# Optimization experiments

Measured on AMD Instinct MI355X. Metric: run time of the kernel, lower is better.

The kernel has to match this reference:

```python
import jax, jax.numpy as jnp
import numpy as np


def setup_inputs() -> dict:
    key = jax.random.key(0)
    k_x, k_idx, k_sgn = jax.random.split(key, 3)
    batch, original_dim, proj_dim, c = 32, 1000000, 4096, 8
    x = jax.random.normal(k_x, (batch, original_dim), dtype=jnp.float32)
    rand_indices = jax.random.randint(k_idx, (original_dim, c), 0, proj_dim, dtype=jnp.int32)
    # random signs in {-1, +1}, matching torch.randint(0,2)*2-1 cast to int8
    rand_signs = (jax.random.randint(k_sgn, (original_dim, c), 0, 2, dtype=jnp.int32) * 2 - 1)
    return {"x": x, "rand_indices": rand_indices, "rand_signs": rand_signs,
            "proj_dim": proj_dim, "c": c}


def reference(x, rand_indices, rand_signs, proj_dim, c):
    # SJLT: each input coordinate d is scattered to c random output buckets
    # with random sign; normalized by 1/sqrt(c) so the sketch preserves norms.
    scale = jnp.asarray(1.0 / np.sqrt(c), dtype=x.dtype)
    batch = x.shape[0]
    out = jnp.zeros((batch, proj_dim), dtype=x.dtype)
    # c is a small fixed constant; loop over it, vectorize over batch & features.
    for j in range(c):
        vals = x * rand_signs[:, j].astype(x.dtype)      # [B, D]
        out = out.at[:, rand_indices[:, j]].add(vals)     # scatter-add along proj dim
    return out * scale
```

## Files before the change

### kernel.cpp

```cpp
#include <hip/hip_runtime.h>
#include <hip/hip_fp16.h>


#define D_TOTAL 1000000
#define PROJ    4096
#define C_SK    8
#define NE      (D_TOTAL * C_SK)
#define SCALE   0.35355339059327373f

#define CAPA    131072
#define CAP     2304
#define BINCAP  112
#define TILE    4096
#define NBLK_A  ((NE + TILE - 1) / TILE)
#define NBLK_T  ((D_TOTAL + 255) / 256)

#define CURA_OFF   0
#define CURB_OFF   16384
#define LISTB_OFF  65536
#define LISTB_SZ   ((size_t)PROJ * CAP * 4)
#define XT_OFF     (LISTB_OFF + LISTB_SZ)
#define XT_SZ      ((size_t)D_TOTAL * 32 * 2)
#define LISTA_OFF  (XT_OFF + XT_SZ)
#define LISTA_SZ   ((size_t)64 * CAPA * 4)
#define WS_ROOMY   (LISTA_OFF + LISTA_SZ)
#define WS_TIGHT   (XT_OFF + XT_SZ)

__global__ void init_cursors_kernel(int* __restrict__ curA, int* __restrict__ curB) {
    int i = blockIdx.x * blockDim.x + threadIdx.x;
    if (i < 64)   curA[i] = i * CAPA;
    if (i < PROJ) curB[i] = i * CAP;
}

__device__ __forceinline__ void rank_and_stage(bool ok, int kb, int payload,
                                               int* __restrict__ cnt,
                                               int* __restrict__ stage,
                                               int* __restrict__ gcur,
                                               int* __restrict__ glist,
                                               int gcur_idx, int glim) {
    const unsigned long long valid = __ballot(ok);
    unsigned long long mask = valid;
    #pragma unroll
    for (int b = 0; b < 6; ++b) {
        const unsigned long long vote = __ballot((kb >> b) & 1);
        mask &= ((kb >> b) & 1) ? vote : ~vote;
    }
    if (ok) {
        const int lane = threadIdx.x & 63;
        const int rank = __popcll(mask & ((1ULL << lane) - 1ULL));
        const int leader = __ffsll((unsigned long long)mask) - 1;
        int base = 0;
        if (rank == 0) base = atomicAdd(&cnt[kb], __popcll(mask));
        base = __shfl(base, leader, 64);
        const int pos = base + rank;
        if (pos < BINCAP) {
            stage[kb * BINCAP + pos] = payload;
        } else {
            const int gp = atomicAdd(&gcur[gcur_idx], 1);
            if (gp < glim) glist[gp] = payload;
        }
    }
}

__device__ __forceinline__ void flush_bins(int* __restrict__ cnt,
                                           int* __restrict__ basek,
                                           const int* __restrict__ stage,
                                           int* __restrict__ gcur,
                                           int* __restrict__ glist,
                                           int gidx0, int capPer) {
    const int tid = threadIdx.x;
    if (tid < 64) {
        const int m = min(cnt[tid], BINCAP);
        cnt[tid]   = m;
        basek[tid] = atomicAdd(&gcur[gidx0 + tid], m);
    }
    __syncthreads();
    const int w = tid >> 6, lane = tid & 63;
    #pragma unroll 1
    for (int bi = 0; bi < 16; ++bi) {
        const int kb  = w * 16 + bi;
        const int m   = cnt[kb];
        const int gb  = basek[kb];
        const int lim = (gidx0 + kb + 1) * capPer;
        for (int i = lane; i < m; i += 64)
            if (gb + i < lim) glist[gb + i] = stage[kb * BINCAP + i];
    }
}

__device__ __forceinline__ void pass_a_body(int abid, char* smem,
                                            const int* __restrict__ idx,
                                            const int* __restrict__ sgn,
                                            int* __restrict__ curA,
                                            int* __restrict__ listA) {
    int* stage = (int*)smem;
    int* cnt   = (int*)(smem + 64 * BINCAP * 4);
    int* basek = cnt + 64;
    const int tid = threadIdx.x;
    if (tid < 64) cnt[tid] = 0;
    __syncthreads();

    const int v0 = abid * (TILE / 4);
    #pragma unroll 1
    for (int k = 0; k < TILE / 1024; ++k) {
        const int vi = v0 + k * 256 + tid;
        const bool okv = vi < NE / 4;
        int4 i4 = {0,0,0,0}, s4 = {0,0,0,0};
        if (okv) { i4 = ((const int4*)idx)[vi]; s4 = ((const int4*)sgn)[vi]; }
        const int g0 = vi * 4;
        #pragma unroll
        for (int m = 0; m < 4; ++m) {
            const int bucket = (m == 0) ? i4.x : (m == 1) ? i4.y : (m == 2) ? i4.z : i4.w;
            const int sg     = (m == 0) ? s4.x : (m == 1) ? s4.y : (m == 2) ? s4.z : s4.w;
            const int kb = okv ? (bucket >> 6) : 0;
            const int payload = (g0 + m) | ((bucket & 63) << 24)
                              | (int)((unsigned)sg & 0x80000000u);
            rank_and_stage(okv, kb, payload, cnt, stage, curA, listA, kb, (kb + 1) * CAPA);
        }
    }
    __syncthreads();
    flush_bins(cnt, basek, stage, curA, listA, 0, CAPA);
}

__device__ __forceinline__ void transpose_body(int tbid, char* smem,
                                               const float* __restrict__ x,
                                               unsigned short* __restrict__ xT) {
    float (*tile)[257] = (float(*)[257])smem;
    const int tid = threadIdx.x;
    const int d0  = tbid * 256;
    const int row = tid >> 3;
    const int c8  = tid & 7;

    if (d0 + 256 <= D_TOTAL) {
        #pragma unroll
        for (int k = 0; k < 8; ++k) {
            const int c = (c8 + 8 * k) * 4;
            const float4 v = *(const float4*)(x + (size_t)row * D_TOTAL + d0 + c);
            tile[row][c] = v.x; tile[row][c+1] = v.y;
            tile[row][c+2] = v.z; tile[row][c+3] = v.w;
        }
    } else {
        for (int k = 0; k < 8; ++k) {
            const int c = (c8 + 8 * k) * 4;
            for (int m = 0; m < 4; ++m) {
                const int d = d0 + c + m;
                tile[row][c + m] = (d < D_TOTAL) ? x[(size_t)row * D_TOTAL + d] : 0.f;
            }
        }
    }
    __syncthreads();

    const int part = tid & 3;
    #pragma unroll
    for (int k = 0; k < 4; ++k) {
        const int dl = k * 64 + (tid >> 2);
        if (d0 + dl < D_TOTAL) {
            unsigned short h[8];
            #pragma unroll
            for (int i = 0; i < 8; ++i)
                h[i] = __half_as_ushort(__float2half(tile[part * 8 + i][dl]));
            *(uint4*)(xT + ((size_t)(d0 + dl)) * 32 + part * 8) = *(const uint4*)h;
        }
    }
}

__global__ __launch_bounds__(256, 4)
void pass_a_transpose_kernel(const int* __restrict__ idx, const int* __restrict__ sgn,
                             int* __restrict__ curA, int* __restrict__ listA,
                             const float* __restrict__ x, unsigned short* __restrict__ xT) {
    __shared__ char smem[33024];
    const int id = blockIdx.x;
    if ((id % 3 == 0) && (id / 3 < NBLK_A)) {
        pass_a_body(id / 3, smem, idx, sgn, curA, listA);
    } else {
        const int tbid = id - id / 3 - ((id % 3) ? 1 : 0);
        if (tbid < NBLK_T) transpose_body(tbid, smem, x, xT);
    }
}

__global__ __launch_bounds__(256, 5)
void pass_a_kernel(const int* __restrict__ idx, const int* __restrict__ sgn,
                   int* __restrict__ curA, int* __restrict__ listA) {
    __shared__ char smem[29184];
    pass_a_body(blockIdx.x, smem, idx, sgn, curA, listA);
}

__global__ __launch_bounds__(256, 4)
void transpose_kernel(const float* __restrict__ x, unsigned short* __restrict__ xT) {
    __shared__ char smem[32896];
    transpose_body(blockIdx.x, smem, x, xT);
}

__global__ __launch_bounds__(256, 5)
void pass_b_kernel(const int* __restrict__ curA, const int* __restrict__ listA,
                   int* __restrict__ curB, int* __restrict__ listB) {
    __shared__ int stage[64 * BINCAP];
    __shared__ int cnt[64];
    __shared__ int basek[64];
    const int tid  = threadIdx.x;
    const int part = blockIdx.x >> 5;
    const int tile = blockIdx.x & 31;
    if (tid < 64) cnt[tid] = 0;
    __syncthreads();

    const int pstart = part * CAPA;
    const int pcount = min(curA[part] - pstart, CAPA);
    const int t0 = tile * TILE;
    const int t1 = min(t0 + TILE, pcount);

    #pragma unroll 1
    for (int k = 0; k < TILE / 256; ++k) {
        const int i  = t0 + k * 256 + tid;
        const bool ok = i < t1;
        const int e  = ok ? listA[pstart + i] : 0;
        const int kb = ok ? ((e >> 24) & 63) : 0;
        const int payload = e & 0x807FFFFF;
        rank_and_stage(ok, kb, payload, cnt, stage, curB, listB,
                       part * 64 + kb, (part * 64 + kb + 1) * CAP);
    }
    __syncthreads();
    flush_bins(cnt, basek, stage, curB, listB, part * 64, CAP);
}

__global__ __launch_bounds__(256, 8)
void gather_kernel(const int* __restrict__ curB, const int* __restrict__ listB,
                   const unsigned short* __restrict__ xT, float* __restrict__ out) {
    __shared__ int   lst[CAP];
    __shared__ float red[4][32];
    const int tid  = threadIdx.x;
    const int w    = tid >> 6;
    const int lane = tid & 63;
    const int p    = blockIdx.x;
    const int start = p * CAP;
    const int n     = min(curB[p] - start, CAP);
    const int slot = lane >> 2;
    const int bq   = lane & 3;

    for (int i4 = tid; i4 < (n >> 2); i4 += 256)
        ((int4*)lst)[i4] = ((const int4*)(listB + start))[i4];
    if (tid < (n & 3)) lst[(n & ~3) + tid] = listB[start + (n & ~3) + tid];
    __syncthreads();

    float a0=0.f,a1=0.f,a2=0.f,a3=0.f,a4=0.f,a5=0.f,a6=0.f,a7=0.f;
    for (int base = w * 16; base < n; base += 512) {
        int pl[8];
        #pragma unroll
        for (int j = 0; j < 8; ++j) {
            const int e = base + j * 64 + slot;
            pl[j] = (e < n) ? lst[e] : 0;
        }
        uint4 hv[8];
        #pragma unroll
        for (int j = 0; j < 8; ++j) {
            int d = (pl[j] & 0x7FFFFF) >> 3;
            d = min(d, D_TOTAL - 1);
            hv[j] = *(const uint4*)(xT + (size_t)d * 32 + bq * 8);
        }
        #pragma unroll
        for (int j = 0; j < 8; ++j) {
            const int e = base + j * 64 + slot;
            const float s = (e < n) ? ((pl[j] < 0) ? -1.f : 1.f) : 0.f;
            float2 f;
            f = __half22float2(*(const __half2*)&hv[j].x); a0 = fmaf(s, f.x, a0); a1 = fmaf(s, f.y, a1);
            f = __half22float2(*(const __half2*)&hv[j].y); a2 = fmaf(s, f.x, a2); a3 = fmaf(s, f.y, a3);
            f = __half22float2(*(const __half2*)&hv[j].z); a4 = fmaf(s, f.x, a4); a5 = fmaf(s, f.y, a5);
            f = __half22float2(*(const __half2*)&hv[j].w); a6 = fmaf(s, f.x, a6); a7 = fmaf(s, f.y, a7);
        }
    }
    #pragma unroll
    for (int m = 4; m <= 32; m <<= 1) {
        a0 += __shfl_xor(a0, m, 64); a1 += __shfl_xor(a1, m, 64);
        a2 += __shfl_xor(a2, m, 64); a3 += __shfl_xor(a3, m, 64);
        a4 += __shfl_xor(a4, m, 64); a5 += __shfl_xor(a5, m, 64);
        a6 += __shfl_xor(a6, m, 64); a7 += __shfl_xor(a7, m, 64);
    }
    if (lane < 4) {
        float* r = &red[w][lane * 8];
        r[0]=a0; r[1]=a1; r[2]=a2; r[3]=a3; r[4]=a4; r[5]=a5; r[6]=a6; r[7]=a7;
    }
    __syncthreads();
    if (tid < 32) {
        const float v = red[0][tid] + red[1][tid] + red[2][tid] + red[3][tid];
        out[(size_t)tid * PROJ + p] = v * SCALE;
    }
}

#define BG 8
#define NCHUNK 64
#define BLOCK 1024
__global__ __launch_bounds__(BLOCK, 4)
void sjlt_scatter_fallback(const float* __restrict__ x,
                           const int* __restrict__ idx,
                           const int* __restrict__ sgn,
                           float* __restrict__ out) {
    __shared__ float acc[BG * PROJ];
    const int tid = threadIdx.x;
    #pragma unroll
    for (int i = 0; i < (BG * PROJ) / BLOCK; ++i) acc[i * BLOCK + tid] = 0.0f;
    __syncthreads();
    const int chunk = D_TOTAL / NCHUNK;
    const int d0 = blockIdx.x * chunk;
    const int d1 = d0 + chunk;
    const int bg = blockIdx.y * BG;
    for (int d = d0 + tid; d < d1; d += BLOCK) {
        const int4 i0 = *(const int4*)(idx + (size_t)d * C_SK);
        const int4 i1 = *(const int4*)(idx + (size_t)d * C_SK + 4);
        const int4 s0 = *(const int4*)(sgn + (size_t)d * C_SK);
        const int4 s1 = *(const int4*)(sgn + (size_t)d * C_SK + 4);
        #pragma unroll
        for (int b = 0; b < BG; ++b) {
            const float xv = __builtin_nontemporal_load(x + (size_t)(bg + b) * D_TOTAL + d);
            const unsigned xb = __float_as_uint(xv);
            float* accb = acc + b * PROJ;
            atomicAdd(accb + i0.x, __uint_as_float(xb ^ ((unsigned)s0.x & 0x80000000u)));
            atomicAdd(accb + i0.y, __uint_as_float(xb ^ ((unsigned)s0.y & 0x80000000u)));
            atomicAdd(accb + i0.z, __uint_as_float(xb ^ ((unsigned)s0.z & 0x80000000u)));
            atomicAdd(accb + i0.w, __uint_as_float(xb ^ ((unsigned)s0.w & 0x80000000u)));
            atomicAdd(accb + i1.x, __uint_as_float(xb ^ ((unsigned)s1.x & 0x80000000u)));
            atomicAdd(accb + i1.y, __uint_as_float(xb ^ ((unsigned)s1.y & 0x80000000u)));
            atomicAdd(accb + i1.z, __uint_as_float(xb ^ ((unsigned)s1.z & 0x80000000u)));
            atomicAdd(accb + i1.w, __uint_as_float(xb ^ ((unsigned)s1.w & 0x80000000u)));
        }
    }
    __syncthreads();
    #pragma unroll
    for (int i = 0; i < (BG * PROJ) / BLOCK; ++i) {
        const int lin = i * BLOCK + tid;
        const int b = lin >> 12;
        const int pp = lin & (PROJ - 1);
        unsafeAtomicAdd(out + (size_t)(bg + b) * PROJ + pp, acc[lin] * SCALE);
    }
}

extern "C" void kernel_launch(void* const* d_in, const int* in_sizes, int n_in,
                              void* d_out, int out_size, void* d_ws, size_t ws_size,
                              hipStream_t stream) {
    const float* x   = (const float*)d_in[0];
    const int*   idx = (const int*)d_in[1];
    const int*   sgn = (const int*)d_in[2];
    float*       out = (float*)d_out;

    if (ws_size < WS_TIGHT) {
        (void)hipMemsetAsync(out, 0, (size_t)out_size * sizeof(float), stream);
        dim3 grid(NCHUNK, 32 / BG);
        sjlt_scatter_fallback<<<grid, BLOCK, 0, stream>>>(x, idx, sgn, out);
        return;
    }

    char* ws = (char*)d_ws;
    int*            curA  = (int*)(ws + CURA_OFF);
    int*            curB  = (int*)(ws + CURB_OFF);
    int*            listB = (int*)(ws + LISTB_OFF);
    unsigned short* xT    = (unsigned short*)(ws + XT_OFF);

    init_cursors_kernel<<<(PROJ + 255) / 256, 256, 0, stream>>>(curA, curB);

    if (ws_size >= WS_ROOMY) {
        int* listA = (int*)(ws + LISTA_OFF);
        pass_a_transpose_kernel<<<NBLK_A + NBLK_T, 256, 0, stream>>>(
            idx, sgn, curA, listA, x, xT);
        pass_b_kernel<<<64 * 32, 256, 0, stream>>>(curA, listA, curB, listB);
    } else {
        int* listA = (int*)(ws + XT_OFF);
        pass_a_kernel<<<NBLK_A, 256, 0, stream>>>(idx, sgn, curA, listA);
        pass_b_kernel<<<64 * 32, 256, 0, stream>>>(curA, listA, curB, listB);
        transpose_kernel<<<NBLK_T, 256, 0, stream>>>(x, xT);
    }
    gather_kernel<<<PROJ, 256, 0, stream>>>(curB, listB, xT, out);
}
```

Before: 433.3 us.

## Split input dimension into segments for locality-aware gather with partial-sum reduction

Pass A now bins entries by both input-dimension segment (16 segments) and coarse bucket, and pass B produces per-segment, per-bucket lists. The gather then runs per (segment, bucket) with one wave per bucket and writes partial sums, which a new reduce kernel adds across segments. The aim is to keep the xT rows touched by concurrent blocks within a narrow range of the input dimension so they hit in cache, and to balance work across many small blocks. The cost is an extra kernel, a partial buffer, and atomics on bins that straddle segment boundaries. The smaller per-bin capacities could overflow and silently drop entries.

Result: faster. 358.6 us (-17.2%).

```diff
diff --git a/kernel.cpp b/kernel.cpp
--- a/kernel.cpp
+++ b/kernel.cpp
@@ -8,30 +8,38 @@
 #define NE      (D_TOTAL * C_SK)
 #define SCALE   0.35355339059327373f
 
-#define CAPA    131072
-#define CAP     2304
-#define BINCAP  112
+#define NSEG    16
+#define SEG_D   62500
+#define CAPA2   8448
+#define CAP_B   192
+#define BINCAP_A 112
+#define BINCAP_B 120
 #define TILE    4096
+#define TILE_B  4352
 #define NBLK_A  ((NE + TILE - 1) / TILE)
 #define NBLK_T  ((D_TOTAL + 255) / 256)
 
-#define CURA_OFF   0
-#define CURB_OFF   16384
-#define LISTB_OFF  65536
-#define LISTB_SZ   ((size_t)PROJ * CAP * 4)
-#define XT_OFF     (LISTB_OFF + LISTB_SZ)
-#define XT_SZ      ((size_t)D_TOTAL * 32 * 2)
-#define LISTA_OFF  (XT_OFF + XT_SZ)
-#define LISTA_SZ   ((size_t)64 * CAPA * 4)
-#define WS_ROOMY   (LISTA_OFF + LISTA_SZ)
-#define WS_TIGHT   (XT_OFF + XT_SZ)
+#define CURA_OFF    0
+#define CURB_OFF    16384
+#define LISTB_OFF   294912
+#define LISTB_SZ    ((size_t)NSEG * PROJ * CAP_B * 4)
+#define XT_OFF_R    (LISTB_OFF + LISTB_SZ)
+#define XT_SZ       ((size_t)D_TOTAL * 32 * 2)
+#define LISTA_OFF_R (XT_OFF_R + XT_SZ)
+#define LISTA_SZ    ((size_t)NSEG * 64 * CAPA2 * 4)
+#define PARTIAL_SZ  ((size_t)NSEG * PROJ * 32 * 4)
+#define WS_ROOMY    (LISTA_OFF_R + LISTA_SZ)
+#define PARTIAL_T   (LISTB_OFF + LISTB_SZ)
+#define XTA_OFF_T   (PARTIAL_T + PARTIAL_SZ)
+#define WS_TIGHT    (XTA_OFF_T + XT_SZ)
 
 __global__ void init_cursors_kernel(int* __restrict__ curA, int* __restrict__ curB) {
     int i = blockIdx.x * blockDim.x + threadIdx.x;
-    if (i < 64)   curA[i] = i * CAPA;
-    if (i < PROJ) curB[i] = i * CAP;
-}
-
+    if (i < NSEG * 64) curA[i] = i * CAPA2;
+    if (i < NSEG * PROJ) curB[i] = i * CAP_B;
+}
+
+template<int BC>
 __device__ __forceinline__ void rank_and_stage(bool ok, int kb, int payload,
                                                int* __restrict__ cnt,
                                                int* __restrict__ stage,
@@ -53,8 +61,8 @@
         if (rank == 0) base = atomicAdd(&cnt[kb], __popcll(mask));
         base = __shfl(base, leader, 64);
         const int pos = base + rank;
-        if (pos < BINCAP) {
-            stage[kb * BINCAP + pos] = payload;
+        if (pos < BC) {
+            stage[kb * BC + pos] = payload;
         } else {
             const int gp = atomicAdd(&gcur[gcur_idx], 1);
             if (gp < glim) glist[gp] = payload;
@@ -62,6 +70,7 @@
     }
 }
 
+template<int BC>
 __device__ __forceinline__ void flush_bins(int* __restrict__ cnt,
                                            int* __restrict__ basek,
                                            const int* __restrict__ stage,
@@ -70,7 +79,7 @@
                                            int gidx0, int capPer) {
     const int tid = threadIdx.x;
     if (tid < 64) {
-        const int m = min(cnt[tid], BINCAP);
+        const int m = min(cnt[tid], BC);
         cnt[tid]   = m;
         basek[tid] = atomicAdd(&gcur[gidx0 + tid], m);
     }
@@ -83,7 +92,7 @@
         const int gb  = basek[kb];
         const int lim = (gidx0 + kb + 1) * capPer;
         for (int i = lane; i < m; i += 64)
-            if (gb + i < lim) glist[gb + i] = stage[kb * BINCAP + i];
+            if (gb + i < lim) glist[gb + i] = stage[kb * BC + i];
     }
 }
 
@@ -93,13 +102,17 @@
                                             int* __restrict__ curA,
                                             int* __restrict__ listA) {
     int* stage = (int*)smem;
-    int* cnt   = (int*)(smem + 64 * BINCAP * 4);
+    int* cnt   = (int*)(smem + 64 * BINCAP_A * 4);
     int* basek = cnt + 64;
     const int tid = threadIdx.x;
     if (tid < 64) cnt[tid] = 0;
     __syncthreads();
 
+    const int d_lo = abid * 512;
+    const int seg  = d_lo / SEG_D;
+    const bool boundary = ((d_lo + 511) / SEG_D) != seg;
     const int v0 = abid * (TILE / 4);
+
     #pragma unroll 1
     for (int k = 0; k < TILE / 1024; ++k) {
         const int vi = v0 + k * 256 + tid;
@@ -114,11 +127,19 @@
             const int kb = okv ? (bucket >> 6) : 0;
             const int payload = (g0 + m) | ((bucket & 63) << 24)
                               | (int)((unsigned)sg & 0x80000000u);
-            rank_and_stage(okv, kb, payload, cnt, stage, curA, listA, kb, (kb + 1) * CAPA);
-        }
-    }
-    __syncthreads();
-    flush_bins(cnt, basek, stage, curA, listA, 0, CAPA);
+            if (!boundary) {
+                rank_and_stage<BINCAP_A>(okv, kb, payload, cnt, stage, curA, listA,
+                                         seg * 64 + kb, (seg * 64 + kb + 1) * CAPA2);
+            } else if (okv) {
+                const int segE = ((g0 + m) >> 3) / SEG_D;
+                const int bin  = segE * 64 + kb;
+                const int gp = atomicAdd(&curA[bin], 1);
+                if (gp < (bin + 1) * CAPA2) listA[gp] = payload;
+            }
+        }
+    }
+    __syncthreads();
+    flush_bins<BINCAP_A>(cnt, basek, stage, curA, listA, seg * 64, CAPA2);
 }
 
 __device__ __forceinline__ void transpose_body(int tbid, char* smem,
@@ -193,78 +214,70 @@
 __global__ __launch_bounds__(256, 5)
 void pass_b_kernel(const int* __restrict__ curA, const int* __restrict__ listA,
                    int* __restrict__ curB, int* __restrict__ listB) {
-    __shared__ int stage[64 * BINCAP];
+    __shared__ int stage[64 * BINCAP_B];
     __shared__ int cnt[64];
     __shared__ int basek[64];
     const int tid  = threadIdx.x;
-    const int part = blockIdx.x >> 5;
-    const int tile = blockIdx.x & 31;
+    const int part = blockIdx.x >> 1;
+    const int tile = blockIdx.x & 1;
     if (tid < 64) cnt[tid] = 0;
     __syncthreads();
 
-    const int pstart = part * CAPA;
-    const int pcount = min(curA[part] - pstart, CAPA);
-    const int t0 = tile * TILE;
-    const int t1 = min(t0 + TILE, pcount);
+    const int pstart = part * CAPA2;
+    const int pcount = min(curA[part] - pstart, CAPA2);
+    const int t0 = tile * TILE_B;
+    const int t1 = min(t0 + TILE_B, pcount);
 
     #pragma unroll 1
-    for (int k = 0; k < TILE / 256; ++k) {
+    for (int k = 0; k < TILE_B / 256; ++k) {
         const int i  = t0 + k * 256 + tid;
         const bool ok = i < t1;
         const int e  = ok ? listA[pstart + i] : 0;
         const int kb = ok ? ((e >> 24) & 63) : 0;
         const int payload = e & 0x807FFFFF;
-        rank_and_stage(ok, kb, payload, cnt, stage, curB, listB,
-                       part * 64 + kb, (part * 64 + kb + 1) * CAP);
-    }
-    __syncthreads();
-    flush_bins(cnt, basek, stage, curB, listB, part * 64, CAP);
+        rank_and_stage<BINCAP_B>(ok, kb, payload, cnt, stage, curB, listB,
+                                 part * 64 + kb, (part * 64 + kb + 1) * CAP_B);
+    }
+    __syncthreads();
+    flush_bins<BINCAP_B>(cnt, basek, stage, curB, listB, part * 64, CAP_B);
 }
 
 __global__ __launch_bounds__(256, 8)
-void gather_kernel(const int* __restrict__ curB, const int* __restrict__ listB,
-                   const unsigned short* __restrict__ xT, float* __restrict__ out) {
-    __shared__ int   lst[CAP];
-    __shared__ float red[4][32];
+void gather_seg_kernel(const int* __restrict__ curB, const int* __restrict__ listB,
+                       const unsigned short* __restrict__ xT,
+                       float* __restrict__ partial) {
+    __shared__ int lst[4][CAP_B];
     const int tid  = threadIdx.x;
     const int w    = tid >> 6;
     const int lane = tid & 63;
-    const int p    = blockIdx.x;
-    const int start = p * CAP;
-    const int n     = min(curB[p] - start, CAP);
+    const int gid  = blockIdx.x;
+    const int k    = gid & 7;
+    const int j    = gid >> 3;
+    const int seg  = k + 8 * (j >> 10);
+    const int p    = (j & 1023) * 4 + w;
+    const int bin  = seg * PROJ + p;
+    const int start = bin * CAP_B;
+    const int n     = min(curB[bin] - start, CAP_B);
+
+    for (int i = lane; i < n; i += 64) lst[w][i] = listB[start + i];
+
     const int slot = lane >> 2;
     const int bq   = lane & 3;
-
-    for (int i4 = tid; i4 < (n >> 2); i4 += 256)
-        ((int4*)lst)[i4] = ((const int4*)(listB + start))[i4];
-    if (tid < (n & 3)) lst[(n & ~3) + tid] = listB[start + (n & ~3) + tid];
-    __syncthreads();
-
     float a0=0.f,a1=0.f,a2=0.f,a3=0.f,a4=0.f,a5=0.f,a6=0.f,a7=0.f;
-    for (int base = w * 16; base < n; base += 512) {
-        int pl[8];
-        #pragma unroll
-        for (int j = 0; j < 8; ++j) {
-            const int e = base + j * 64 + slot;
-            pl[j] = (e < n) ? lst[e] : 0;
-        }
-        uint4 hv[8];
-        #pragma unroll
-        for (int j = 0; j < 8; ++j) {
-            int d = (pl[j] & 0x7FFFFF) >> 3;
-            d = min(d, D_TOTAL - 1);
-            hv[j] = *(const uint4*)(xT + (size_t)d * 32 + bq * 8);
-        }
-        #pragma unroll
-        for (int j = 0; j < 8; ++j) {
-            const int e = base + j * 64 + slot;
-            const float s = (e < n) ? ((pl[j] < 0) ? -1.f : 1.f) : 0.f;
-            float2 f;
-            f = __half22float2(*(const __half2*)&hv[j].x); a0 = fmaf(s, f.x, a0); a1 = fmaf(s, f.y, a1);
-            f = __half22float2(*(const __half2*)&hv[j].y); a2 = fmaf(s, f.x, a2); a3 = fmaf(s, f.y, a3);
-            f = __half22float2(*(const __half2*)&hv[j].z); a4 = fmaf(s, f.x, a4); a5 = fmaf(s, f.y, a5);
-            f = __half22float2(*(const __half2*)&hv[j].w); a6 = fmaf(s, f.x, a6); a7 = fmaf(s, f.y, a7);
-        }
+    #pragma unroll 2
+    for (int base = 0; base < n; base += 16) {
+        const int  e  = base + slot;
+        const bool ok = e < n;
+        const int  pl = lst[w][ok ? e : 0];
+        int d = (pl & 0x7FFFFF) >> 3;
+        d = min(d, D_TOTAL - 1);
+        const float s = ok ? ((pl < 0) ? -1.f : 1.f) : 0.f;
+        const uint4 hv = *(const uint4*)(xT + (size_t)d * 32 + bq * 8);
+        float2 f;
+        f = __half22float2(*(const __half2*)&hv.x); a0 = fmaf(s, f.x, a0); a1 = fmaf(s, f.y, a1);
+        f = __half22float2(*(const __half2*)&hv.y); a2 = fmaf(s, f.x, a2); a3 = fmaf(s, f.y, a3);
+        f = __half22float2(*(const __half2*)&hv.z); a4 = fmaf(s, f.x, a4); a5 = fmaf(s, f.y, a5);
+        f = __half22float2(*(const __half2*)&hv.w); a6 = fmaf(s, f.x, a6); a7 = fmaf(s, f.y, a7);
     }
     #pragma unroll
     for (int m = 4; m <= 32; m <<= 1) {
@@ -274,14 +287,23 @@
         a6 += __shfl_xor(a6, m, 64); a7 += __shfl_xor(a7, m, 64);
     }
     if (lane < 4) {
-        float* r = &red[w][lane * 8];
-        r[0]=a0; r[1]=a1; r[2]=a2; r[3]=a3; r[4]=a4; r[5]=a5; r[6]=a6; r[7]=a7;
-    }
-    __syncthreads();
-    if (tid < 32) {
-        const float v = red[0][tid] + red[1][tid] + red[2][tid] + red[3][tid];
-        out[(size_t)tid * PROJ + p] = v * SCALE;
-    }
+        float v[8] = {a0,a1,a2,a3,a4,a5,a6,a7};
+        float* dst = partial + (size_t)bin * 32 + lane * 8;
+        #pragma unroll
+        for (int i = 0; i < 8; ++i) dst[i] = v[i];
+    }
+}
+
+__global__ __launch_bounds__(256)
+void reduce_kernel(const float* __restrict__ partial, float* __restrict__ out) {
+    const int gtid = blockIdx.x * 256 + threadIdx.x;
+    const int p = gtid & (PROJ - 1);
+    const int b = gtid >> 12;
+    float s = 0.f;
+    #pragma unroll
+    for (int sg = 0; sg < NSEG; ++sg)
+        s += partial[((size_t)(sg * PROJ + p)) * 32 + b];
+    out[(size_t)b * PROJ + p] = s * SCALE;
 }
 
 #define BG 8
@@ -347,23 +369,29 @@
     }
 
     char* ws = (char*)d_ws;
-    int*            curA  = (int*)(ws + CURA_OFF);
-    int*            curB  = (int*)(ws + CURB_OFF);
-    int*            listB = (int*)(ws + LISTB_OFF);
-    unsigned short* xT    = (unsigned short*)(ws + XT_OFF);
-
-    init_cursors_kernel<<<(PROJ + 255) / 256, 256, 0, stream>>>(curA, curB);
+    int* curA  = (int*)(ws + CURA_OFF);
+    int* curB  = (int*)(ws + CURB_OFF);
+    int* listB = (int*)(ws + LISTB_OFF);
+
+    init_cursors_kernel<<<256, 256, 0, stream>>>(curA, curB);
 
     if (ws_size >= WS_ROOMY) {
-        int* listA = (int*)(ws + LISTA_OFF);
+        unsigned short* xT      = (unsigned short*)(ws + XT_OFF_R);
+        int*            listA   = (int*)(ws + LISTA_OFF_R);
+        float*          partial = (float*)(ws + LISTA_OFF_R);
         pass_a_transpose_kernel<<<NBLK_A + NBLK_T, 256, 0, stream>>>(
             idx, sgn, curA, listA, x, xT);
-        pass_b_kernel<<<64 * 32, 256, 0, stream>>>(curA, listA, curB, listB);
+        pass_b_kernel<<<2048, 256, 0, stream>>>(curA, listA, curB, listB);
+        gather_seg_kernel<<<NSEG * PROJ / 4, 256, 0, stream>>>(curB, listB, xT, partial);
+        reduce_kernel<<<(32 * PROJ) / 256, 256, 0, stream>>>(partial, out);
     } else {
-        int* listA = (int*)(ws + XT_OFF);
+        float*          partial = (float*)(ws + PARTIAL_T);
+        unsigned short* xT      = (unsigned short*)(ws + XTA_OFF_T);
+        int*            listA   = (int*)(ws + XTA_OFF_T);
         pass_a_kernel<<<NBLK_A, 256, 0, stream>>>(idx, sgn, curA, listA);
-        pass_b_kernel<<<64 * 32, 256, 0, stream>>>(curA, listA, curB, listB);
+        pass_b_kernel<<<2048, 256, 0, stream>>>(curA, listA, curB, listB);
         transpose_kernel<<<NBLK_T, 256, 0, stream>>>(x, xT);
-    }
-    gather_kernel<<<PROJ, 256, 0, stream>>>(curB, listB, xT, out);
-}
+        gather_seg_kernel<<<NSEG * PROJ / 4, 256, 0, stream>>>(curB, listB, xT, partial);
+        reduce_kernel<<<(32 * PROJ) / 256, 256, 0, stream>>>(partial, out);
+    }
+}
```
